# Optimization experiments

Measured on AMD Instinct MI355X. Metric: run time of the kernel, lower is better.

The kernel has to match this reference:

```python
import jax, jax.numpy as jnp
import numpy as np

N, E = 50000, 400000
IN, HID, HEADS, OUT, EDIM = 128, 16, 8, 128, 32


def _lin(key, fan_in, fan_out, bias=True):
    k1, k2 = jax.random.split(key)
    s = 1.0 / np.sqrt(fan_in)
    W = jax.random.uniform(k1, (fan_in, fan_out), jnp.float32, -s, s)
    if bias:
        b = jax.random.uniform(k2, (fan_out,), jnp.float32, -s, s)
        return W, b
    return W


def setup_inputs() -> dict:
    key = jax.random.key(0)
    ks = jax.random.split(key, 16)
    x = jax.random.normal(ks[0], (N, IN), jnp.float32)
    edge_index = jax.random.randint(ks[1], (2, E), 0, N, jnp.int64)
    edge_feats = jax.random.normal(ks[2], (E, EDIM), jnp.float32)
    H1 = HEADS * HID  # 128
    Wq1, bq1 = _lin(ks[3], IN, H1)
    Wk1, bk1 = _lin(ks[4], IN, H1)
    Wv1, bv1 = _lin(ks[5], IN, H1)
    We1 = _lin(ks[6], EDIM, H1, bias=False)
    Ws1, bs1 = _lin(ks[7], IN, H1)
    Wq2, bq2 = _lin(ks[8], H1, OUT)
    Wk2, bk2 = _lin(ks[9], H1, OUT)
    Wv2, bv2 = _lin(ks[10], H1, OUT)
    We2 = _lin(ks[11], EDIM, OUT, bias=False)
    Ws2, bs2 = _lin(ks[12], H1, OUT)
    return dict(x=x, edge_index=edge_index, edge_feats=edge_feats,
                Wq1=Wq1, bq1=bq1, Wk1=Wk1, bk1=bk1, Wv1=Wv1, bv1=bv1, We1=We1, Ws1=Ws1, bs1=bs1,
                Wq2=Wq2, bq2=bq2, Wk2=Wk2, bk2=bk2, Wv2=Wv2, bv2=bv2, We2=We2, Ws2=Ws2, bs2=bs2)


def transformer_conv(x, src, dst, e, Wq, bq, Wk, bk, Wv, bv, We, Ws, bs, heads, ch, concat):
    # PyG TransformerConv: project at nodes, gather to edges.
    n = x.shape[0]
    q = (x @ Wq + bq).reshape(n, heads, ch)[dst]          # [E,H,C]
    k = (x @ Wk + bk).reshape(n, heads, ch)[src]
    v = (x @ Wv + bv).reshape(n, heads, ch)[src]
    ee = (e @ We).reshape(-1, heads, ch)                   # edge conditioning
    k = k + ee
    v = v + ee
    alpha = (q * k).sum(-1) / jnp.sqrt(jnp.asarray(ch, x.dtype))  # [E,H]
    # per-destination segment softmax
    m = jax.ops.segment_max(alpha, dst, num_segments=n)
    m = jnp.where(jnp.isfinite(m), m, 0.0)
    ea = jnp.exp(alpha - m[dst])
    denom = jax.ops.segment_sum(ea, dst, num_segments=n)
    attn = ea / jnp.maximum(denom[dst], 1e-16)
    out = jax.ops.segment_sum(attn[:, :, None] * v, dst, num_segments=n)  # [N,H,C]
    out = out.reshape(n, heads * ch) if concat else out.mean(axis=1)
    return out + x @ Ws + bs  # root_weight skip


def reference(x, edge_index, edge_feats,
              Wq1, bq1, Wk1, bk1, Wv1, bv1, We1, Ws1, bs1,
              Wq2, bq2, Wk2, bk2, Wv2, bv2, We2, Ws2, bs2):
    src, dst = edge_index[0], edge_index[1]
    h = jax.nn.relu(transformer_conv(x, src, dst, edge_feats,
                                     Wq1, bq1, Wk1, bk1, Wv1, bv1, We1, Ws1, bs1,
                                     HEADS, HID, True))
    # dropout p=0.0 (eval) -> identity
    out = jax.nn.relu(transformer_conv(h, src, dst, edge_feats,
                                       Wq2, bq2, Wk2, bk2, Wv2, bv2, We2, Ws2, bs2,
                                       1, OUT, False))
    return out
```

## Files before the change

### kernel.cpp

```cpp
#include <hip/hip_runtime.h>


using u16 = unsigned short;
using u32 = unsigned int;

#define NODES 50000
#define EDGES 400000
#define NB196 196

typedef __attribute__((ext_vector_type(8))) short bf16x8;
typedef __attribute__((ext_vector_type(4))) float f32x4;

__device__ __forceinline__ float bflo(u32 u) { return __uint_as_float(u << 16); }
__device__ __forceinline__ float bfhi(u32 u) { return __uint_as_float(u & 0xffff0000u); }
__device__ __forceinline__ u16 f2bf(float f) {
    u32 u = __float_as_uint(f);
    u += 0x7fffu + ((u >> 16) & 1u);
    return (u16)(u >> 16);
}
__device__ __forceinline__ u32 pack2(float a, float b) {
    return (u32)f2bf(a) | ((u32)f2bf(b) << 16);
}
__device__ __forceinline__ float rdv(const void* p, int i, int f) {
    return f ? ((const float*)p)[i]
             : __uint_as_float(((u32) reinterpret_cast<const u16*>(p)[i]) << 16);
}

#if __has_builtin(__builtin_amdgcn_fdot2_f32_bf16)
typedef __attribute__((ext_vector_type(2))) __bf16 bf2;
__device__ __forceinline__ float dot2bf(u32 a, u32 b, float c) {
    return __builtin_amdgcn_fdot2_f32_bf16(__builtin_bit_cast(bf2, a),
                                           __builtin_bit_cast(bf2, b), c, false);
}
#else
__device__ __forceinline__ float dot2bf(u32 a, u32 b, float c) {
    return fmaf(bflo(a), bflo(b), fmaf(bfhi(a), bfhi(b), c));
}
#endif

__device__ __forceinline__ float fexp2(float x) {
#if __has_builtin(__builtin_amdgcn_exp2f)
    return __builtin_amdgcn_exp2f(x);
#else
    return exp2f(x);
#endif
}

template <int CTRL>
__device__ __forceinline__ float dpp_addf(float x) {
    int y = __builtin_amdgcn_update_dpp(0, __float_as_int(x), CTRL, 0xF, 0xF, true);
    return x + __int_as_float(y);
}
template <int GRP>
__device__ __forceinline__ float grp_sum(float p, int lane) {
    p = dpp_addf<0xB1>(p);
    p = dpp_addf<0x4E>(p);
    p = dpp_addf<0x141>(p);
    if (GRP == 64) {
        p = dpp_addf<0x140>(p);
        p += __int_as_float(__builtin_amdgcn_ds_swizzle(__float_as_int(p), 0x401F));
        p += __int_as_float(__builtin_amdgcn_ds_bpermute((lane ^ 32) << 2,
                                                         __float_as_int(p)));
    }
    return p;
}

template <int SRC>
__device__ __forceinline__ u32 bcast8u(u32 x) {
    return (u32)__builtin_amdgcn_ds_swizzle((int)x, 0x18 | (SRC << 5));
}

__global__ __launch_bounds__(256) void fill_sentinel(float* __restrict__ out, int n, float val) {
    int i = blockIdx.x * 256 + threadIdx.x;
    if (i < n) out[i] = val;
}

__global__ __launch_bounds__(64) void detect_fmt(const u32* __restrict__ xw,
                                                 const int* __restrict__ eraw,
                                                 int* __restrict__ flags) {
    int lane = threadIdx.x;
    u32 e = (xw[lane] >> 7) & 0xffu;
    unsigned long long sane = __ballot(e >= 90u && e <= 141u);
    unsigned long long zodd = __ballot(eraw[1 + 2 * lane] == 0);
    if (lane == 0) {
        flags[0] = (sane == ~0ull) ? 0 : 1;
        flags[1] = (zodd == ~0ull) ? 1 : 0;
    }
}

#define CXB 3125
#define CDB 1563
__global__ __launch_bounds__(256) void convert_count(
    const void* __restrict__ X, const int* __restrict__ raw,
    const int* __restrict__ flags, u16* __restrict__ xbf,
    int* __restrict__ deg, int total, int E) {
    int b = blockIdx.x;
    if (b < CXB) {
        int i = (b * 256 + threadIdx.x) * 8;
        if (i >= total) return;
        if (flags[0]) {
            const float* xf = (const float*)X + i;
            float4 lo = *reinterpret_cast<const float4*>(xf);
            float4 hi = *reinterpret_cast<const float4*>(xf + 4);
            uint4 val = make_uint4(pack2(lo.x, lo.y), pack2(lo.z, lo.w),
                                   pack2(hi.x, hi.y), pack2(hi.z, hi.w));
            *reinterpret_cast<uint4*>(xbf + i) = val;
        } else {
            *reinterpret_cast<uint4*>(xbf + i) =
                *reinterpret_cast<const uint4*>((const u16*)X + i);
        }
    } else {
        int e = (b - CXB) * 256 + threadIdx.x;
        if (e < E) {
            int f = flags[1];
            int d = f ? raw[2 * (E + e)] : raw[E + e];
            if ((unsigned)d < (unsigned)NODES) atomicAdd(&deg[d], 1);
        }
    }
}

struct TPtrs {
    const void* src[8];
    u16*        dst[8];
    int         K[8];
};
struct WqeP {
    const void *Wq1, *We1, *bq1, *Wq2, *We2, *bq2;
    u16 *WtA, *WtB, *Wt2;
    float *bqe1, *bqe2;
    uint2 *WeP1, *WeP2;
};

__global__ __launch_bounds__(256) void prep_w(TPtrs P, WqeP Q, const int* __restrict__ flags) {
    int f = flags[0];
    int b = blockIdx.x;
    if (b < 32) {
        int m = b >> 2;
        int K = P.K[m];
        int quarter = (K * 128) >> 2;
        u16* d = P.dst[m];
        int base = (b & 3) * quarter;
        const float* sf = (const float*)P.src[m];
        const u16*   sb = (const u16*)P.src[m];
        for (int idx = base + threadIdx.x; idx < base + quarter; idx += 256) {
            int k = idx >> 7, n = idx & 127;
            d[n * K + k] = f ? f2bf(sf[idx]) : sb[idx];
        }
        return;
    }
    int idx = (b - 32) * 256 + threadIdx.x;
    if (idx < 32768) {
        int col = idx >> 7, i = idx & 127;
        int hh = col >> 5, d = col & 31;
        float s = 0.f;
#pragma unroll
        for (int c = 0; c < 16; ++c)
            s += rdv(Q.Wq1, i * 128 + hh * 16 + c, f) * rdv(Q.We1, d * 128 + hh * 16 + c, f);
        if (col < 128) Q.WtA[col * 128 + i] = f2bf(s);
        else           Q.WtB[(col - 128) * 128 + i] = f2bf(s);
    } else if (idx < 49152) {
        int t = idx - 32768;
        int col = t >> 7, i = t & 127;
        float s = 0.f;
        if (col < 32) {
            for (int c = 0; c < 128; ++c)
                s += rdv(Q.Wq2, i * 128 + c, f) * rdv(Q.We2, col * 128 + c, f);
        }
        Q.Wt2[col * 128 + i] = f2bf(s * 0.125f);
    } else if (idx < 49408) {
        int col = idx - 49152;
        int hh = col >> 5, d = col & 31;
        float s = 0.f;
#pragma unroll
        for (int c = 0; c < 16; ++c)
            s += rdv(Q.bq1, hh * 16 + c, f) * rdv(Q.We1, d * 128 + hh * 16 + c, f);
        Q.bqe1[col] = s;
    } else if (idx < 49536) {
        int d = idx - 49408;
        float s = 0.f;
        if (d < 32)
            for (int c = 0; c < 128; ++c)
                s += rdv(Q.bq2, c, f) * rdv(Q.We2, d * 128 + c, f);
        Q.bqe2[d] = s * 0.125f;
    } else if (idx < 50560) {
        int ent = idx - 49536;
        int t = ent >> 6, l = ent & 63, c0 = 2 * l;
        u32 xv = pack2(rdv(Q.We1, (2 * t) * 128 + c0, f),
                       rdv(Q.We1, (2 * t + 1) * 128 + c0, f));
        u32 yv = pack2(rdv(Q.We1, (2 * t) * 128 + c0 + 1, f),
                       rdv(Q.We1, (2 * t + 1) * 128 + c0 + 1, f));
        Q.WeP1[ent] = make_uint2(xv, yv);
    } else if (idx < 51584) {
        int ent = idx - 50560;
        int t = ent >> 6, l = ent & 63, c0 = 2 * l;
        u32 xv = pack2(rdv(Q.We2, (2 * t) * 128 + c0, f),
                       rdv(Q.We2, (2 * t + 1) * 128 + c0, f));
        u32 yv = pack2(rdv(Q.We2, (2 * t) * 128 + c0 + 1, f),
                       rdv(Q.We2, (2 * t + 1) * 128 + c0 + 1, f));
        Q.WeP2[ent] = make_uint2(xv, yv);
    }
}

__device__ __forceinline__ int block_scan256(int v) {
    __shared__ int ws[4];
    int t = threadIdx.x, lane = t & 63, w = t >> 6;
    int x = v;
#pragma unroll
    for (int off = 1; off < 64; off <<= 1) {
        int y = __shfl_up(x, off, 64);
        if (lane >= off) x += y;
    }
    if (lane == 63) ws[w] = x;
    __syncthreads();
#pragma unroll
    for (int j = 0; j < 3; ++j)
        if (j < w) x += ws[j];
    return x;
}

__global__ __launch_bounds__(256) void scan_a(const int* __restrict__ deg,
                                              int* __restrict__ bsum, int n) {
    int i = blockIdx.x * 256 + threadIdx.x;
    int v = (i < n) ? deg[i] : 0;
    int incl = block_scan256(v);
    if (threadIdx.x == 255) bsum[blockIdx.x] = incl;
}

__global__ __launch_bounds__(256) void scan_b(int* __restrict__ bsum, int nb) {
    int t = threadIdx.x;
    int v = (t < nb) ? bsum[t] : 0;
    int incl = block_scan256(v);
    if (t < nb) bsum[t] = incl - v;
}

__global__ __launch_bounds__(256) void scan_c(const int* __restrict__ deg,
                                              const int* __restrict__ bsum,
                                              int* __restrict__ row_ptr,
                                              int* __restrict__ cursor, int n) {
    int b = blockIdx.x;
    int i = b * 256 + threadIdx.x;
    int v = (i < n) ? deg[i] : 0;
    int incl = block_scan256(v) + bsum[b];
    if (i < n) {
        row_ptr[i + 1] = incl;
        cursor[i] = incl - v;
    }
    if (i == 0) row_ptr[0] = 0;
}

__global__ __launch_bounds__(256) void fill_csr(const int* __restrict__ raw,
                                                const int* __restrict__ flags,
                                                int* __restrict__ cursor,
                                                int* __restrict__ srcs,
                                                int* __restrict__ eids, int E) {
    int e = blockIdx.x * 256 + threadIdx.x;
    if (e < E) {
        int f = flags[1];
        int d = f ? raw[2 * (E + e)] : raw[E + e];
        int s = f ? raw[2 * e] : raw[e];
        if ((unsigned)d < (unsigned)NODES && (unsigned)s < (unsigned)NODES) {
            int pos = atomicAdd(&cursor[d], 1);
            if ((unsigned)pos < (unsigned)E) { srcs[pos] = s; eids[pos] = e; }
        }
    }
}

__global__ __launch_bounds__(256) void gather_ef(const int* __restrict__ eids,
                                                 const void* __restrict__ EF,
                                                 const int* __restrict__ flags,
                                                 u16* __restrict__ EFG, int E) {
    int t = blockIdx.x * 256 + threadIdx.x;
    int pos = t >> 2, seg = t & 3;
    if (pos >= E) return;
    int e = eids[pos];
    uint4 val;
    if (flags[0]) {
        const float* src = (const float*)EF + (size_t)e * 32 + seg * 8;
        float4 lo = *reinterpret_cast<const float4*>(src);
        float4 hi = *reinterpret_cast<const float4*>(src + 4);
        val = make_uint4(pack2(lo.x, lo.y), pack2(lo.z, lo.w),
                         pack2(hi.x, hi.y), pack2(hi.z, hi.w));
    } else {
        val = *reinterpret_cast<const uint4*>((const u16*)EF + (size_t)e * 32 + seg * 8);
    }
    *reinterpret_cast<uint4*>(EFG + (size_t)pos * 32 + seg * 8) = val;
}

struct GemmSets {
    const u16*  Wt[6];
    const void* bias[6];
    u16*        O[6];
    int         bf32[6];
    int         pitch[6];
    float       oscale[6];
};

__global__ __launch_bounds__(256) void gemm128(
    const u16* __restrict__ A, const int* __restrict__ flags, GemmSets S, int M) {
    constexpr int K = 128;
    constexpr int PAD = K + 8;
    constexpr int KV = K / 8;
    __shared__ u16 Asl[64 * PAD];
    __shared__ u16 Bsl[128 * PAD];

    const u16*  Wt   = S.Wt[blockIdx.y];
    const void* bias = S.bias[blockIdx.y];
    u16*        O    = S.O[blockIdx.y];
    int pitch = S.pitch[blockIdx.y];
    float os  = S.oscale[blockIdx.y];
    int f = S.bf32[blockIdx.y] ? 1 : flags[0];
    int m0 = blockIdx.x * 64;

    for (int idx = threadIdx.x; idx < 64 * KV; idx += 256) {
        int r = idx / KV, cv = idx % KV;
        int gr = m0 + r;
        uint4 val = make_uint4(0, 0, 0, 0);
        if (gr < M) val = *reinterpret_cast<const uint4*>(A + (size_t)gr * K + cv * 8);
        *reinterpret_cast<uint4*>(&Asl[r * PAD + cv * 8]) = val;
    }
    for (int idx = threadIdx.x; idx < 128 * KV; idx += 256) {
        int r = idx / KV, cv = idx % KV;
        *reinterpret_cast<uint4*>(&Bsl[r * PAD + cv * 8]) =
            *reinterpret_cast<const uint4*>(Wt + r * K + cv * 8);
    }
    __syncthreads();

    int lane = threadIdx.x & 63, wv = threadIdx.x >> 6;
    int l15 = lane & 15;
    int quad = lane >> 4;
    int kq = quad * 8;

    f32x4 b4[8];
#pragma unroll
    for (int nt = 0; nt < 8; ++nt) {
        int col0 = nt * 16 + quad * 4;
        if (bias) {
            if (f) {
                b4[nt] = *reinterpret_cast<const f32x4*>((const float*)bias + col0);
            } else {
                uint2 bu = *reinterpret_cast<const uint2*>((const u16*)bias + col0);
                b4[nt][0] = bflo(bu.x); b4[nt][1] = bfhi(bu.x);
                b4[nt][2] = bflo(bu.y); b4[nt][3] = bfhi(bu.y);
            }
        } else {
            b4[nt][0] = b4[nt][1] = b4[nt][2] = b4[nt][3] = 0.f;
        }
    }

    f32x4 acc[8] = {};
#pragma unroll
    for (int k0 = 0; k0 < K; k0 += 32) {
        bf16x8 xf = *reinterpret_cast<const bf16x8*>(&Asl[(wv * 16 + l15) * PAD + k0 + kq]);
#pragma unroll
        for (int nt = 0; nt < 8; ++nt) {
            bf16x8 wf = *reinterpret_cast<const bf16x8*>(&Bsl[(nt * 16 + l15) * PAD + k0 + kq]);
            acc[nt] = __builtin_amdgcn_mfma_f32_16x16x32_bf16(wf, xf, acc[nt], 0, 0, 0);
        }
    }

    int row = m0 + wv * 16 + l15;
    if (row < M) {
        u16* Orow = O + (size_t)row * pitch;
#pragma unroll
        for (int nt = 0; nt < 8; ++nt) {
            uint2 pk;
            pk.x = pack2((acc[nt][0] + b4[nt][0]) * os, (acc[nt][1] + b4[nt][1]) * os);
            pk.y = pack2((acc[nt][2] + b4[nt][2]) * os, (acc[nt][3] + b4[nt][3]) * os);
            *reinterpret_cast<uint2*>(Orow + nt * 16 + quad * 4) = pk;
        }
    }
}

template <int HEADS, int F32OUT>
__global__ __launch_bounds__(256) void attn_kernel(
    const int* __restrict__ row_ptr, const int* __restrict__ srcs,
    const u16* __restrict__ Q, const u16* __restrict__ KV,
    const u16* __restrict__ EFG,
    const u16* __restrict__ QWA, const u16* __restrict__ QWB,
    const u16* __restrict__ SK, const uint2* __restrict__ WeP,
    void* __restrict__ OUT, int nn) {
    int wv = threadIdx.x >> 6, lane = threadIdx.x & 63;
    int node = blockIdx.x * 4 + wv;
    if (node >= nn) return;
    int h = lane >> 3, j = lane & 7;
    int c0 = lane * 2;
    constexpr int GRP = (HEADS == 8) ? 8 : 64;

    u32 qb = *reinterpret_cast<const u32*>(Q + (size_t)node * 128 + c0);
    const u16* qp = (HEADS == 8)
        ? ((h < 4 ? QWA : QWB) + (size_t)node * 128 + (h & 3) * 32 + j * 4)
        : (QWA + (size_t)node * 128 + j * 4);
    uint2 qwu = *reinterpret_cast<const uint2*>(qp);

    int beg = __builtin_amdgcn_readfirstlane(row_ptr[node]);
    int end = __builtin_amdgcn_readfirstlane(row_ptr[node + 1]);

    float l_run = 0.f, a0 = 0.f, a1 = 0.f;
    float f0 = 0.f, f1 = 0.f, f2 = 0.f, f3 = 0.f;

    auto edge_step = [&](u32 kbv, u32 vbv, uint2 ebv, bool valid) {
        float p = dot2bf(qb, kbv,
                 dot2bf(qwu.x, ebv.x,
                 dot2bf(qwu.y, ebv.y, 0.f)));
        p = grp_sum<GRP>(p, lane);
        float w = fexp2(p);
        if (!valid) w = 0.f;
        l_run += w;
        a0 = fmaf(w, bflo(vbv), a0);
        a1 = fmaf(w, bfhi(vbv), a1);
        f0 = fmaf(w, bflo(ebv.x), f0); f1 = fmaf(w, bfhi(ebv.x), f1);
        f2 = fmaf(w, bflo(ebv.y), f2); f3 = fmaf(w, bfhi(ebv.y), f3);
    };

    int i = beg;
    for (; i + 8 <= end; i += 8) {
        u32 kb[8], vb[8]; uint2 eb[8];
#pragma unroll
        for (int t = 0; t < 8; ++t) {
            int s = srcs[i + t];
            const u16* kp = KV + (size_t)s * 256;
            kb[t] = *reinterpret_cast<const u32*>(kp + c0);
            vb[t] = *reinterpret_cast<const u32*>(kp + 128 + c0);
            eb[t] = *reinterpret_cast<const uint2*>(EFG + (size_t)(i + t) * 32 + j * 4);
        }
#pragma unroll
        for (int t = 0; t < 8; ++t) edge_step(kb[t], vb[t], eb[t], true);
    }
    for (; i < end; i += 4) {
        int kleft = end - i;
        u32 kb[4], vb[4]; uint2 eb[4];
#pragma unroll
        for (int t = 0; t < 4; ++t) {
            int idx = (i + t < end) ? i + t : end - 1;
            int s = srcs[idx];
            const u16* kp = KV + (size_t)s * 256;
            kb[t] = *reinterpret_cast<const u32*>(kp + c0);
            vb[t] = *reinterpret_cast<const u32*>(kp + 128 + c0);
            eb[t] = *reinterpret_cast<const uint2*>(EFG + (size_t)idx * 32 + j * 4);
        }
#pragma unroll
        for (int t = 0; t < 4; ++t) edge_step(kb[t], vb[t], eb[t], t < kleft);
    }

    u32 Fp0 = pack2(f0, f1), Fp1 = pack2(f2, f3);
    float acc0 = 0.f, acc1 = 0.f;
#define EPI(SRC) do { \
        u32 A = bcast8u<SRC>(Fp0), B = bcast8u<SRC>(Fp1); \
        uint2 w0 = WeP[(2 * SRC) * 64 + lane]; \
        uint2 w1 = WeP[(2 * SRC + 1) * 64 + lane]; \
        acc0 = dot2bf(A, w0.x, acc0); acc0 = dot2bf(B, w1.x, acc0); \
        acc1 = dot2bf(A, w0.y, acc1); acc1 = dot2bf(B, w1.y, acc1); \
    } while (0)
    EPI(0); EPI(1); EPI(2); EPI(3); EPI(4); EPI(5); EPI(6); EPI(7);
#undef EPI

    float inv = 1.f / fmaxf(l_run, 1e-16f);
    u32 sb = *reinterpret_cast<const u32*>(SK + (size_t)node * 128 + c0);
    float o0 = fmaxf(fmaf(a0 + acc0, inv, bflo(sb)), 0.f);
    float o1 = fmaxf(fmaf(a1 + acc1, inv, bfhi(sb)), 0.f);
    if (F32OUT) {
        *reinterpret_cast<float2*>((float*)OUT + (size_t)node * 128 + c0) =
            make_float2(o0, o1);
    } else {
        *reinterpret_cast<u32*>((u16*)OUT + (size_t)node * 128 + c0) = pack2(o0, o1);
    }
}

extern "C" void kernel_launch(void* const* d_in, const int* in_sizes, int n_in,
                              void* d_out, int out_size, void* d_ws, size_t ws_size,
                              hipStream_t stream) {
    const int N = NODES, E = EDGES;
    const void* x  = d_in[0];
    const int*  ei = (const int*)d_in[1];
    const void* ef = d_in[2];
    const void* Wq1 = d_in[3];  const void* bq1 = d_in[4];
    const void* Wk1 = d_in[5];  const void* bk1 = d_in[6];
    const void* Wv1 = d_in[7];  const void* bv1 = d_in[8];
    const void* We1 = d_in[9];
    const void* Ws1 = d_in[10]; const void* bs1 = d_in[11];
    const void* Wq2 = d_in[12]; const void* bq2 = d_in[13];
    const void* Wk2 = d_in[14]; const void* bk2 = d_in[15];
    const void* Wv2 = d_in[16]; const void* bv2 = d_in[17];
    const void* We2 = d_in[18];
    const void* Ws2 = d_in[19]; const void* bs2 = d_in[20];

    char* ws = (char*)d_ws;
    size_t off = 0;
    auto carve = [&](size_t bytes) -> void* {
        void* p = ws + off;
        off += (bytes + 255) & ~(size_t)255;
        return p;
    };

    u16* WtQ1 = (u16*)carve(128 * 128 * 2);
    u16* WtK1 = (u16*)carve(128 * 128 * 2);
    u16* WtV1 = (u16*)carve(128 * 128 * 2);
    u16* WtS1 = (u16*)carve(128 * 128 * 2);
    u16* WtQ2 = (u16*)carve(128 * 128 * 2);
    u16* WtK2 = (u16*)carve(128 * 128 * 2);
    u16* WtV2 = (u16*)carve(128 * 128 * 2);
    u16* WtS2 = (u16*)carve(128 * 128 * 2);
    u16* WtqA = (u16*)carve(128 * 128 * 2);
    u16* WtqB = (u16*)carve(128 * 128 * 2);
    u16* Wtq2 = (u16*)carve(128 * 128 * 2);
    float* bqe1 = (float*)carve(256 * 4);
    float* bqe2 = (float*)carve(128 * 4);
    uint2* WeP1 = (uint2*)carve(1024 * 8);
    uint2* WeP2 = (uint2*)carve(1024 * 8);
    int* flags   = (int*)carve(256);
    int* deg     = (int*)carve((size_t)N * 4);
    int* bsum    = (int*)carve((size_t)NB196 * 4);
    int* row_ptr = (int*)carve((size_t)(N + 1) * 4);
    int* cursor  = (int*)carve((size_t)N * 4);
    int* srcs    = (int*)carve((size_t)E * 4);
    int* eids    = (int*)carve((size_t)E * 4);
    u16* xbf  = (u16*)carve((size_t)N * 128 * 2);
    u16* q    = (u16*)carve((size_t)N * 128 * 2);
    u16* kv   = (u16*)carve((size_t)N * 256 * 2);
    u16* sk   = (u16*)carve((size_t)N * 128 * 2);
    u16* h    = (u16*)carve((size_t)N * 128 * 2);
    u16* qweA = (u16*)carve((size_t)N * 128 * 2);
    u16* qweB = (u16*)carve((size_t)N * 128 * 2);
    u16* qwe2 = (u16*)carve((size_t)N * 128 * 2);
    u16* efg  = (u16*)carve((size_t)E * 32 * 2);
    const size_t REQ = off;

    if (ws_size < REQ) {
        hipLaunchKernelGGL(fill_sentinel, dim3((out_size + 255) / 256), dim3(256), 0, stream,
                           (float*)d_out, out_size, 16.0f * (float)(ws_size >> 20));
        return;
    }

    const float s2_1 = 0.25f * 1.44269504f;
    const float s2_2 = 0.08838834764831845f * 1.44269504f;

    hipLaunchKernelGGL(detect_fmt, dim3(1), dim3(64), 0, stream, (const u32*)x, ei, flags);

    (void)hipMemsetAsync(deg, 0, (size_t)N * 4, stream);
    hipLaunchKernelGGL(convert_count, dim3(CXB + CDB), dim3(256), 0, stream,
                       x, ei, flags, xbf, deg, N * 128, E);

    TPtrs tp;
    tp.src[0] = Wq1; tp.dst[0] = WtQ1; tp.K[0] = 128;
    tp.src[1] = Wk1; tp.dst[1] = WtK1; tp.K[1] = 128;
    tp.src[2] = Wv1; tp.dst[2] = WtV1; tp.K[2] = 128;
    tp.src[3] = Ws1; tp.dst[3] = WtS1; tp.K[3] = 128;
    tp.src[4] = Wq2; tp.dst[4] = WtQ2; tp.K[4] = 128;
    tp.src[5] = Wk2; tp.dst[5] = WtK2; tp.K[5] = 128;
    tp.src[6] = Wv2; tp.dst[6] = WtV2; tp.K[6] = 128;
    tp.src[7] = Ws2; tp.dst[7] = WtS2; tp.K[7] = 128;
    WqeP wp;
    wp.Wq1 = Wq1; wp.We1 = We1; wp.bq1 = bq1;
    wp.Wq2 = Wq2; wp.We2 = We2; wp.bq2 = bq2;
    wp.WtA = WtqA; wp.WtB = WtqB; wp.Wt2 = Wtq2;
    wp.bqe1 = bqe1; wp.bqe2 = bqe2;
    wp.WeP1 = WeP1; wp.WeP2 = WeP2;
    hipLaunchKernelGGL(prep_w, dim3(32 + 202), dim3(256), 0, stream, tp, wp, flags);

    hipLaunchKernelGGL(scan_a, dim3(NB196), dim3(256), 0, stream, deg, bsum, N);
    hipLaunchKernelGGL(scan_b, dim3(1), dim3(256), 0, stream, bsum, NB196);
    hipLaunchKernelGGL(scan_c, dim3(NB196), dim3(256), 0, stream, deg, bsum, row_ptr, cursor, N);
    hipLaunchKernelGGL(fill_csr, dim3((E + 255) / 256), dim3(256), 0, stream, ei, flags, cursor,
                       srcs, eids, E);

    hipLaunchKernelGGL(gather_ef, dim3(E * 4 / 256), dim3(256), 0, stream,
                       eids, ef, flags, efg, E);

    const int gN = (N + 63) / 64;
    const int gA = (N + 3) / 4;

    {
        GemmSets S;
        S.Wt[0] = WtQ1; S.bias[0] = bq1;  S.O[0] = q;        S.bf32[0] = 0; S.pitch[0] = 128; S.oscale[0] = s2_1;
        S.Wt[1] = WtK1; S.bias[1] = bk1;  S.O[1] = kv;       S.bf32[1] = 0; S.pitch[1] = 256; S.oscale[1] = 1.f;
        S.Wt[2] = WtV1; S.bias[2] = bv1;  S.O[2] = kv + 128; S.bf32[2] = 0; S.pitch[2] = 256; S.oscale[2] = 1.f;
        S.Wt[3] = WtS1; S.bias[3] = bs1;  S.O[3] = sk;       S.bf32[3] = 0; S.pitch[3] = 128; S.oscale[3] = 1.f;
        S.Wt[4] = WtqA; S.bias[4] = bqe1;       S.O[4] = qweA; S.bf32[4] = 1; S.pitch[4] = 128; S.oscale[4] = s2_1;
        S.Wt[5] = WtqB; S.bias[5] = bqe1 + 128; S.O[5] = qweB; S.bf32[5] = 1; S.pitch[5] = 128; S.oscale[5] = s2_1;
        hipLaunchKernelGGL(gemm128, dim3(gN, 6), dim3(256), 0, stream, xbf, flags, S, N);
    }
    hipLaunchKernelGGL((attn_kernel<8, 0>), dim3(gA), dim3(256), 0, stream,
                       row_ptr, srcs, q, kv, efg, qweA, qweB, sk, WeP1, (void*)h, N);

    {
        GemmSets S;
        S.Wt[0] = WtQ2; S.bias[0] = bq2;  S.O[0] = q;        S.bf32[0] = 0; S.pitch[0] = 128; S.oscale[0] = s2_2;
        S.Wt[1] = WtK2; S.bias[1] = bk2;  S.O[1] = kv;       S.bf32[1] = 0; S.pitch[1] = 256; S.oscale[1] = 1.f;
        S.Wt[2] = WtV2; S.bias[2] = bv2;  S.O[2] = kv + 128; S.bf32[2] = 0; S.pitch[2] = 256; S.oscale[2] = 1.f;
        S.Wt[3] = WtS2; S.bias[3] = bs2;  S.O[3] = sk;       S.bf32[3] = 0; S.pitch[3] = 128; S.oscale[3] = 1.f;
        S.Wt[4] = Wtq2; S.bias[4] = bqe2; S.O[4] = qwe2;     S.bf32[4] = 1; S.pitch[4] = 128; S.oscale[4] = s2_2;
        S.Wt[5] = Wtq2; S.bias[5] = bqe2; S.O[5] = qwe2;     S.bf32[5] = 1; S.pitch[5] = 128; S.oscale[5] = s2_2;
        hipLaunchKernelGGL(gemm128, dim3(gN, 5), dim3(256), 0, stream, h, flags, S, N);
    }
    hipLaunchKernelGGL((attn_kernel<1, 1>), dim3(gA), dim3(256), 0, stream,
                       row_ptr, srcs, q, kv, efg, qwe2, qwe2, sk, WeP2, d_out, N);
}
```

Baseline: 429.8 us.

## Process two destination nodes per wavefront with interleaved edge loads

The attention kernel now assigns two adjacent destination nodes to each wavefront and issues their 8-edge gather batches back to back before computing, so more memory requests are in flight per wave. The fixed 8/4 tail loops become a single clamped 8-edge loop with masking, and the edge-weight projection coefficients are loaded once and shared by both nodes' epilogues. In exchange the kernel uses more registers, which can lower occupancy, the grid has half as many waves, and lanes may idle when the two nodes have very different degrees.

```diff
diff --git a/kernel.cpp b/kernel.cpp
--- a/kernel.cpp
+++ b/kernel.cpp
@@ -371,6 +371,10 @@
     }
 }
 
+struct NState {
+    float l, a0, a1, f0, f1, f2, f3;
+};
+
 template <int HEADS, int F32OUT>
 __global__ __launch_bounds__(256) void attn_kernel(
     const int* __restrict__ row_ptr, const int* __restrict__ srcs,
@@ -380,89 +384,160 @@
     const u16* __restrict__ SK, const uint2* __restrict__ WeP,
     void* __restrict__ OUT, int nn) {
     int wv = threadIdx.x >> 6, lane = threadIdx.x & 63;
-    int node = blockIdx.x * 4 + wv;
-    if (node >= nn) return;
+    int w = blockIdx.x * 4 + wv;
+    int nA = w * 2;
+    if (nA >= nn) return;
+    bool hasB = (nA + 1) < nn;
+    int nB = hasB ? nA + 1 : nA;
     int h = lane >> 3, j = lane & 7;
     int c0 = lane * 2;
     constexpr int GRP = (HEADS == 8) ? 8 : 64;
 
-    u32 qb = *reinterpret_cast<const u32*>(Q + (size_t)node * 128 + c0);
-    const u16* qp = (HEADS == 8)
-        ? ((h < 4 ? QWA : QWB) + (size_t)node * 128 + (h & 3) * 32 + j * 4)
-        : (QWA + (size_t)node * 128 + j * 4);
-    uint2 qwu = *reinterpret_cast<const uint2*>(qp);
-
-    int beg = __builtin_amdgcn_readfirstlane(row_ptr[node]);
-    int end = __builtin_amdgcn_readfirstlane(row_ptr[node + 1]);
-
-    float l_run = 0.f, a0 = 0.f, a1 = 0.f;
-    float f0 = 0.f, f1 = 0.f, f2 = 0.f, f3 = 0.f;
-
-    auto edge_step = [&](u32 kbv, u32 vbv, uint2 ebv, bool valid) {
-        float p = dot2bf(qb, kbv,
-                 dot2bf(qwu.x, ebv.x,
-                 dot2bf(qwu.y, ebv.y, 0.f)));
-        p = grp_sum<GRP>(p, lane);
-        float w = fexp2(p);
-        if (!valid) w = 0.f;
-        l_run += w;
-        a0 = fmaf(w, bflo(vbv), a0);
-        a1 = fmaf(w, bfhi(vbv), a1);
-        f0 = fmaf(w, bflo(ebv.x), f0); f1 = fmaf(w, bfhi(ebv.x), f1);
-        f2 = fmaf(w, bflo(ebv.y), f2); f3 = fmaf(w, bfhi(ebv.y), f3);
-    };
-
-    int i = beg;
-    for (; i + 8 <= end; i += 8) {
-        u32 kb[8], vb[8]; uint2 eb[8];
+    int begA = __builtin_amdgcn_readfirstlane(row_ptr[nA]);
+    int endA = __builtin_amdgcn_readfirstlane(row_ptr[nA + 1]);
+    int endB = hasB ? __builtin_amdgcn_readfirstlane(row_ptr[nA + 2]) : endA;
+    int begB = endA;
+
+    u32 qbA = *reinterpret_cast<const u32*>(Q + (size_t)nA * 128 + c0);
+    u32 qbB = *reinterpret_cast<const u32*>(Q + (size_t)nB * 128 + c0);
+    const u16* qpA = (HEADS == 8)
+        ? ((h < 4 ? QWA : QWB) + (size_t)nA * 128 + (h & 3) * 32 + j * 4)
+        : (QWA + (size_t)nA * 128 + j * 4);
+    const u16* qpB = (HEADS == 8)
+        ? ((h < 4 ? QWA : QWB) + (size_t)nB * 128 + (h & 3) * 32 + j * 4)
+        : (QWA + (size_t)nB * 128 + j * 4);
+    uint2 qwuA = *reinterpret_cast<const uint2*>(qpA);
+    uint2 qwuB = *reinterpret_cast<const uint2*>(qpB);
+
+    auto load8 = [&](int ii, int ee, u32* kb, u32* vb, uint2* eb) {
 #pragma unroll
         for (int t = 0; t < 8; ++t) {
-            int s = srcs[i + t];
-            const u16* kp = KV + (size_t)s * 256;
-            kb[t] = *reinterpret_cast<const u32*>(kp + c0);
-            vb[t] = *reinterpret_cast<const u32*>(kp + 128 + c0);
-            eb[t] = *reinterpret_cast<const uint2*>(EFG + (size_t)(i + t) * 32 + j * 4);
-        }
-#pragma unroll
-        for (int t = 0; t < 8; ++t) edge_step(kb[t], vb[t], eb[t], true);
-    }
-    for (; i < end; i += 4) {
-        int kleft = end - i;
-        u32 kb[4], vb[4]; uint2 eb[4];
-#pragma unroll
-        for (int t = 0; t < 4; ++t) {
-            int idx = (i + t < end) ? i + t : end - 1;
+            int idx = ii + t;
+            idx = (idx < ee) ? idx : (ee - 1);
+            idx = (idx < ii) ? ii : idx;
             int s = srcs[idx];
             const u16* kp = KV + (size_t)s * 256;
             kb[t] = *reinterpret_cast<const u32*>(kp + c0);
             vb[t] = *reinterpret_cast<const u32*>(kp + 128 + c0);
             eb[t] = *reinterpret_cast<const uint2*>(EFG + (size_t)idx * 32 + j * 4);
         }
-#pragma unroll
-        for (int t = 0; t < 4; ++t) edge_step(kb[t], vb[t], eb[t], t < kleft);
-    }
-
-    u32 Fp0 = pack2(f0, f1), Fp1 = pack2(f2, f3);
-    float acc0 = 0.f, acc1 = 0.f;
-#define EPI(SRC) do { \
-        u32 A = bcast8u<SRC>(Fp0), B = bcast8u<SRC>(Fp1); \
-        uint2 w0 = WeP[(2 * SRC) * 64 + lane]; \
-        uint2 w1 = WeP[(2 * SRC + 1) * 64 + lane]; \
-        acc0 = dot2bf(A, w0.x, acc0); acc0 = dot2bf(B, w1.x, acc0); \
-        acc1 = dot2bf(A, w0.y, acc1); acc1 = dot2bf(B, w1.y, acc1); \
-    } while (0)
-    EPI(0); EPI(1); EPI(2); EPI(3); EPI(4); EPI(5); EPI(6); EPI(7);
-#undef EPI
-
-    float inv = 1.f / fmaxf(l_run, 1e-16f);
-    u32 sb = *reinterpret_cast<const u32*>(SK + (size_t)node * 128 + c0);
-    float o0 = fmaxf(fmaf(a0 + acc0, inv, bflo(sb)), 0.f);
-    float o1 = fmaxf(fmaf(a1 + acc1, inv, bfhi(sb)), 0.f);
-    if (F32OUT) {
-        *reinterpret_cast<float2*>((float*)OUT + (size_t)node * 128 + c0) =
-            make_float2(o0, o1);
-    } else {
-        *reinterpret_cast<u32*>((u16*)OUT + (size_t)node * 128 + c0) = pack2(o0, o1);
+    };
+    auto comp8 = [&](const u32* kb, const u32* vb, const uint2* eb, int kleft,
+                     u32 qb, uint2 qwu, NState& st) {
+#pragma unroll
+        for (int t = 0; t < 8; ++t) {
+            float p = dot2bf(qb, kb[t],
+                      dot2bf(qwu.x, eb[t].x,
+                      dot2bf(qwu.y, eb[t].y, 0.f)));
+            p = grp_sum<GRP>(p, lane);
+            float ww = fexp2(p);
+            if (t >= kleft) ww = 0.f;
+            st.l += ww;
+            st.a0 = fmaf(ww, bflo(vb[t]), st.a0);
+            st.a1 = fmaf(ww, bfhi(vb[t]), st.a1);
+            st.f0 = fmaf(ww, bflo(eb[t].x), st.f0);
+            st.f1 = fmaf(ww, bfhi(eb[t].x), st.f1);
+            st.f2 = fmaf(ww, bflo(eb[t].y), st.f2);
+            st.f3 = fmaf(ww, bfhi(eb[t].y), st.f3);
+        }
+    };
+
+    NState sA = {0.f, 0.f, 0.f, 0.f, 0.f, 0.f, 0.f};
+    NState sB = {0.f, 0.f, 0.f, 0.f, 0.f, 0.f, 0.f};
+
+    int iA = begA, iB = begB;
+    bool aA = iA < endA;
+    bool aB = hasB && (iB < endB);
+    while (aA || aB) {
+        u32 kbA[8], vbA[8]; uint2 ebA[8];
+        u32 kbB[8], vbB[8]; uint2 ebB[8];
+        if (aA) load8(iA, endA, kbA, vbA, ebA);
+        if (aB) load8(iB, endB, kbB, vbB, ebB);
+        if (aA) {
+            comp8(kbA, vbA, ebA, endA - iA, qbA, qwuA, sA);
+            iA += 8; aA = iA < endA;
+        }
+        if (aB) {
+            comp8(kbB, vbB, ebB, endB - iB, qbB, qwuB, sB);
+            iB += 8; aB = iB < endB;
+        }
+    }
+
+    uint2 wD[16];
+#pragma unroll
+    for (int t = 0; t < 16; ++t) wD[t] = WeP[t * 64 + lane];
+
+    auto epi = [&](const NState& st) -> float2 {
+        u32 Fp0 = pack2(st.f0, st.f1), Fp1 = pack2(st.f2, st.f3);
+        float acc0 = 0.f, acc1 = 0.f;
+        {
+            u32 A_ = bcast8u<0>(Fp0), B_ = bcast8u<0>(Fp1);
+            acc0 = dot2bf(A_, wD[0].x, acc0); acc0 = dot2bf(B_, wD[1].x, acc0);
+            acc1 = dot2bf(A_, wD[0].y, acc1); acc1 = dot2bf(B_, wD[1].y, acc1);
+        }
+        {
+            u32 A_ = bcast8u<1>(Fp0), B_ = bcast8u<1>(Fp1);
+            acc0 = dot2bf(A_, wD[2].x, acc0); acc0 = dot2bf(B_, wD[3].x, acc0);
+            acc1 = dot2bf(A_, wD[2].y, acc1); acc1 = dot2bf(B_, wD[3].y, acc1);
+        }
+        {
+            u32 A_ = bcast8u<2>(Fp0), B_ = bcast8u<2>(Fp1);
+            acc0 = dot2bf(A_, wD[4].x, acc0); acc0 = dot2bf(B_, wD[5].x, acc0);
+            acc1 = dot2bf(A_, wD[4].y, acc1); acc1 = dot2bf(B_, wD[5].y, acc1);
+        }
+        {
+            u32 A_ = bcast8u<3>(Fp0), B_ = bcast8u<3>(Fp1);
+            acc0 = dot2bf(A_, wD[6].x, acc0); acc0 = dot2bf(B_, wD[7].x, acc0);
+            acc1 = dot2bf(A_, wD[6].y, acc1); acc1 = dot2bf(B_, wD[7].y, acc1);
+        }
+        {
+            u32 A_ = bcast8u<4>(Fp0), B_ = bcast8u<4>(Fp1);
+            acc0 = dot2bf(A_, wD[8].x, acc0); acc0 = dot2bf(B_, wD[9].x, acc0);
+            acc1 = dot2bf(A_, wD[8].y, acc1); acc1 = dot2bf(B_, wD[9].y, acc1);
+        }
+        {
+            u32 A_ = bcast8u<5>(Fp0), B_ = bcast8u<5>(Fp1);
+            acc0 = dot2bf(A_, wD[10].x, acc0); acc0 = dot2bf(B_, wD[11].x, acc0);
+            acc1 = dot2bf(A_, wD[10].y, acc1); acc1 = dot2bf(B_, wD[11].y, acc1);
+        }
+        {
+            u32 A_ = bcast8u<6>(Fp0), B_ = bcast8u<6>(Fp1);
+            acc0 = dot2bf(A_, wD[12].x, acc0); acc0 = dot2bf(B_, wD[13].x, acc0);
+            acc1 = dot2bf(A_, wD[12].y, acc1); acc1 = dot2bf(B_, wD[13].y, acc1);
+        }
+        {
+            u32 A_ = bcast8u<7>(Fp0), B_ = bcast8u<7>(Fp1);
+            acc0 = dot2bf(A_, wD[14].x, acc0); acc0 = dot2bf(B_, wD[15].x, acc0);
+            acc1 = dot2bf(A_, wD[14].y, acc1); acc1 = dot2bf(B_, wD[15].y, acc1);
+        }
+        return make_float2(acc0, acc1);
+    };
+
+    {
+        float2 ee2 = epi(sA);
+        float inv = 1.f / fmaxf(sA.l, 1e-16f);
+        u32 sb = *reinterpret_cast<const u32*>(SK + (size_t)nA * 128 + c0);
+        float o0 = fmaxf(fmaf(sA.a0 + ee2.x, inv, bflo(sb)), 0.f);
+        float o1 = fmaxf(fmaf(sA.a1 + ee2.y, inv, bfhi(sb)), 0.f);
+        if (F32OUT) {
+            *reinterpret_cast<float2*>((float*)OUT + (size_t)nA * 128 + c0) =
+                make_float2(o0, o1);
+        } else {
+            *reinterpret_cast<u32*>((u16*)OUT + (size_t)nA * 128 + c0) = pack2(o0, o1);
+        }
+    }
+    if (hasB) {
+        float2 ee2 = epi(sB);
+        float inv = 1.f / fmaxf(sB.l, 1e-16f);
+        u32 sb = *reinterpret_cast<const u32*>(SK + (size_t)nB * 128 + c0);
+        float o0 = fmaxf(fmaf(sB.a0 + ee2.x, inv, bflo(sb)), 0.f);
+        float o1 = fmaxf(fmaf(sB.a1 + ee2.y, inv, bfhi(sb)), 0.f);
+        if (F32OUT) {
+            *reinterpret_cast<float2*>((float*)OUT + (size_t)nB * 128 + c0) =
+                make_float2(o0, o1);
+        } else {
+            *reinterpret_cast<u32*>((u16*)OUT + (size_t)nB * 128 + c0) = pack2(o0, o1);
+        }
     }
 }
 
@@ -567,7 +642,7 @@
                        eids, ef, flags, efg, E);
 
     const int gN = (N + 63) / 64;
-    const int gA = (N + 3) / 4;
+    const int gA = (N + 7) / 8;
 
     {
         GemmSets S;
```

New measurement: 447.9 us. 1.04x slower.

## Fuse preprocessing kernels into one cooperative persistent kernel with grid syncs

Applied to the files above, without the earlier changes.

Replaces the chain of small preprocessing launches (format detect, memset, convert/count, weight prep, three-phase scan, CSR fill, edge-feature gather) with a single cooperative kernel of 512 blocks that uses grid-wide syncs between phases. This removes per-launch overhead and inter-kernel gaps for the many tiny kernels. Grid syncs add their own cost, and a fixed 512-block grid with grid-stride loops may use the GPU less evenly than the original per-phase grids. The old multi-launch path is kept as a fallback if the cooperative launch fails.

```diff
diff --git a/kernel.cpp b/kernel.cpp
--- a/kernel.cpp
+++ b/kernel.cpp
@@ -1,5 +1,8 @@
 #include <hip/hip_runtime.h>
-
+#include <hip/hip_cooperative_groups.h>
+
+
+namespace cg = cooperative_groups;
 
 using u16 = unsigned short;
 using u32 = unsigned int;
@@ -7,6 +10,7 @@
 #define NODES 50000
 #define EDGES 400000
 #define NB196 196
+#define COOPG 512
 
 typedef __attribute__((ext_vector_type(8))) short bf16x8;
 typedef __attribute__((ext_vector_type(4))) float f32x4;
@@ -73,50 +77,6 @@
 __global__ __launch_bounds__(256) void fill_sentinel(float* __restrict__ out, int n, float val) {
     int i = blockIdx.x * 256 + threadIdx.x;
     if (i < n) out[i] = val;
-}
-
-__global__ __launch_bounds__(64) void detect_fmt(const u32* __restrict__ xw,
-                                                 const int* __restrict__ eraw,
-                                                 int* __restrict__ flags) {
-    int lane = threadIdx.x;
-    u32 e = (xw[lane] >> 7) & 0xffu;
-    unsigned long long sane = __ballot(e >= 90u && e <= 141u);
-    unsigned long long zodd = __ballot(eraw[1 + 2 * lane] == 0);
-    if (lane == 0) {
-        flags[0] = (sane == ~0ull) ? 0 : 1;
-        flags[1] = (zodd == ~0ull) ? 1 : 0;
-    }
-}
-
-#define CXB 3125
-#define CDB 1563
-__global__ __launch_bounds__(256) void convert_count(
-    const void* __restrict__ X, const int* __restrict__ raw,
-    const int* __restrict__ flags, u16* __restrict__ xbf,
-    int* __restrict__ deg, int total, int E) {
-    int b = blockIdx.x;
-    if (b < CXB) {
-        int i = (b * 256 + threadIdx.x) * 8;
-        if (i >= total) return;
-        if (flags[0]) {
-            const float* xf = (const float*)X + i;
-            float4 lo = *reinterpret_cast<const float4*>(xf);
-            float4 hi = *reinterpret_cast<const float4*>(xf + 4);
-            uint4 val = make_uint4(pack2(lo.x, lo.y), pack2(lo.z, lo.w),
-                                   pack2(hi.x, hi.y), pack2(hi.z, hi.w));
-            *reinterpret_cast<uint4*>(xbf + i) = val;
-        } else {
-            *reinterpret_cast<uint4*>(xbf + i) =
-                *reinterpret_cast<const uint4*>((const u16*)X + i);
-        }
-    } else {
-        int e = (b - CXB) * 256 + threadIdx.x;
-        if (e < E) {
-            int f = flags[1];
-            int d = f ? raw[2 * (E + e)] : raw[E + e];
-            if ((unsigned)d < (unsigned)NODES) atomicAdd(&deg[d], 1);
-        }
-    }
 }
 
 struct TPtrs {
@@ -131,24 +91,7 @@
     uint2 *WeP1, *WeP2;
 };
 
-__global__ __launch_bounds__(256) void prep_w(TPtrs P, WqeP Q, const int* __restrict__ flags) {
-    int f = flags[0];
-    int b = blockIdx.x;
-    if (b < 32) {
-        int m = b >> 2;
-        int K = P.K[m];
-        int quarter = (K * 128) >> 2;
-        u16* d = P.dst[m];
-        int base = (b & 3) * quarter;
-        const float* sf = (const float*)P.src[m];
-        const u16*   sb = (const u16*)P.src[m];
-        for (int idx = base + threadIdx.x; idx < base + quarter; idx += 256) {
-            int k = idx >> 7, n = idx & 127;
-            d[n * K + k] = f ? f2bf(sf[idx]) : sb[idx];
-        }
-        return;
-    }
-    int idx = (b - 32) * 256 + threadIdx.x;
+__device__ __forceinline__ void wqe_item(const WqeP& Q, int idx, int f) {
     if (idx < 32768) {
         int col = idx >> 7, i = idx & 127;
         int hh = col >> 5, d = col & 31;
@@ -216,6 +159,185 @@
     for (int j = 0; j < 3; ++j)
         if (j < w) x += ws[j];
     return x;
+}
+
+struct CoopArgs {
+    const void* X;
+    const int*  raw;
+    const void* EF;
+    TPtrs tp;
+    WqeP  wq;
+    int* flags;
+    int* deg; int* bsum; int* row_ptr; int* cursor;
+    int* srcs; int* eids;
+    u16* xbf; u16* efg;
+};
+
+__global__ __launch_bounds__(256) void coop_prep(CoopArgs A) {
+    cg::grid_group grid = cg::this_grid();
+    const int gid = blockIdx.x * 256 + threadIdx.x;
+    const int gsz = gridDim.x * 256;
+    const int lane = threadIdx.x & 63;
+    const int N = NODES, E = EDGES;
+
+    u32 ew = (((const u32*)A.X)[lane] >> 7) & 0xffu;
+    unsigned long long sane = __ballot(ew >= 90u && ew <= 141u);
+    unsigned long long zodd = __ballot(A.raw[1 + 2 * lane] == 0);
+    const int f  = (sane == ~0ull) ? 0 : 1;
+    const int f1 = (zodd == ~0ull) ? 1 : 0;
+    if (gid == 0) { A.flags[0] = f; A.flags[1] = f1; }
+
+    for (int i = gid; i < N; i += gsz) A.deg[i] = 0;
+    __threadfence();
+    grid.sync();
+
+    for (int i = gid; i < N * 128 / 8; i += gsz) {
+        int o = i * 8;
+        if (f) {
+            const float* xf = (const float*)A.X + o;
+            float4 lo = *reinterpret_cast<const float4*>(xf);
+            float4 hi = *reinterpret_cast<const float4*>(xf + 4);
+            *reinterpret_cast<uint4*>(A.xbf + o) =
+                make_uint4(pack2(lo.x, lo.y), pack2(lo.z, lo.w),
+                           pack2(hi.x, hi.y), pack2(hi.z, hi.w));
+        } else {
+            *reinterpret_cast<uint4*>(A.xbf + o) =
+                *reinterpret_cast<const uint4*>((const u16*)A.X + o);
+        }
+    }
+    for (int e = gid; e < E; e += gsz) {
+        int d = f1 ? A.raw[2 * (E + e)] : A.raw[E + e];
+        if ((unsigned)d < (unsigned)N) atomicAdd(&A.deg[d], 1);
+    }
+    for (int t = gid; t < 8 * 16384; t += gsz) {
+        int m = t >> 14, idx = t & 16383;
+        int k = idx >> 7, n = idx & 127;
+        const float* sf = (const float*)A.tp.src[m];
+        const u16*   sb = (const u16*)A.tp.src[m];
+        A.tp.dst[m][n * 128 + k] = f ? f2bf(sf[idx]) : sb[idx];
+    }
+    for (int idx = gid; idx < 51584; idx += gsz) wqe_item(A.wq, idx, f);
+    __threadfence();
+    grid.sync();
+
+    for (int c = blockIdx.x; c < NB196; c += gridDim.x) {
+        int i = c * 256 + threadIdx.x;
+        int v = (i < N) ? A.deg[i] : 0;
+        int incl = block_scan256(v);
+        if (threadIdx.x == 255) A.bsum[c] = incl;
+    }
+    __threadfence();
+    grid.sync();
+
+    if (blockIdx.x == 0) {
+        int t = threadIdx.x;
+        int v = (t < NB196) ? A.bsum[t] : 0;
+        int incl = block_scan256(v);
+        if (t < NB196) A.bsum[t] = incl - v;
+    }
+    __threadfence();
+    grid.sync();
+
+    for (int c = blockIdx.x; c < NB196; c += gridDim.x) {
+        int i = c * 256 + threadIdx.x;
+        int v = (i < N) ? A.deg[i] : 0;
+        int incl = block_scan256(v) + A.bsum[c];
+        if (i < N) { A.row_ptr[i + 1] = incl; A.cursor[i] = incl - v; }
+        if (i == 0) A.row_ptr[0] = 0;
+    }
+    __threadfence();
+    grid.sync();
+
+    for (int e = gid; e < E; e += gsz) {
+        int d = f1 ? A.raw[2 * (E + e)] : A.raw[E + e];
+        int s = f1 ? A.raw[2 * e] : A.raw[e];
+        if ((unsigned)d < (unsigned)N && (unsigned)s < (unsigned)N) {
+            int pos = atomicAdd(&A.cursor[d], 1);
+            if ((unsigned)pos < (unsigned)E) { A.srcs[pos] = s; A.eids[pos] = e; }
+        }
+    }
+    __threadfence();
+    grid.sync();
+
+    for (int t = gid; t < E * 4; t += gsz) {
+        int pos = t >> 2, seg = t & 3;
+        int e = A.eids[pos];
+        uint4 val;
+        if (f) {
+            const float* src = (const float*)A.EF + (size_t)e * 32 + seg * 8;
+            float4 lo = *reinterpret_cast<const float4*>(src);
+            float4 hi = *reinterpret_cast<const float4*>(src + 4);
+            val = make_uint4(pack2(lo.x, lo.y), pack2(lo.z, lo.w),
+                             pack2(hi.x, hi.y), pack2(hi.z, hi.w));
+        } else {
+            val = *reinterpret_cast<const uint4*>((const u16*)A.EF + (size_t)e * 32 + seg * 8);
+        }
+        *reinterpret_cast<uint4*>(A.efg + (size_t)pos * 32 + seg * 8) = val;
+    }
+}
+
+__global__ __launch_bounds__(64) void detect_fmt(const u32* __restrict__ xw,
+                                                 const int* __restrict__ eraw,
+                                                 int* __restrict__ flags) {
+    int lane = threadIdx.x;
+    u32 e = (xw[lane] >> 7) & 0xffu;
+    unsigned long long sane = __ballot(e >= 90u && e <= 141u);
+    unsigned long long zodd = __ballot(eraw[1 + 2 * lane] == 0);
+    if (lane == 0) {
+        flags[0] = (sane == ~0ull) ? 0 : 1;
+        flags[1] = (zodd == ~0ull) ? 1 : 0;
+    }
+}
+
+#define CXB 3125
+#define CDB 1563
+__global__ __launch_bounds__(256) void convert_count(
+    const void* __restrict__ X, const int* __restrict__ raw,
+    const int* __restrict__ flags, u16* __restrict__ xbf,
+    int* __restrict__ deg, int total, int E) {
+    int b = blockIdx.x;
+    if (b < CXB) {
+        int i = (b * 256 + threadIdx.x) * 8;
+        if (i >= total) return;
+        if (flags[0]) {
+            const float* xf = (const float*)X + i;
+            float4 lo = *reinterpret_cast<const float4*>(xf);
+            float4 hi = *reinterpret_cast<const float4*>(xf + 4);
+            uint4 val = make_uint4(pack2(lo.x, lo.y), pack2(lo.z, lo.w),
+                                   pack2(hi.x, hi.y), pack2(hi.z, hi.w));
+            *reinterpret_cast<uint4*>(xbf + i) = val;
+        } else {
+            *reinterpret_cast<uint4*>(xbf + i) =
+                *reinterpret_cast<const uint4*>((const u16*)X + i);
+        }
+    } else {
+        int e = (b - CXB) * 256 + threadIdx.x;
+        if (e < E) {
+            int f = flags[1];
+            int d = f ? raw[2 * (E + e)] : raw[E + e];
+            if ((unsigned)d < (unsigned)NODES) atomicAdd(&deg[d], 1);
+        }
+    }
+}
+
+__global__ __launch_bounds__(256) void prep_w(TPtrs P, WqeP Q, const int* __restrict__ flags) {
+    int f = flags[0];
+    int b = blockIdx.x;
+    if (b < 32) {
+        int m = b >> 2;
+        int quarter = 16384 >> 2;
+        u16* d = P.dst[m];
+        int base = (b & 3) * quarter;
+        const float* sf = (const float*)P.src[m];
+        const u16*   sb = (const u16*)P.src[m];
+        for (int idx = base + threadIdx.x; idx < base + quarter; idx += 256) {
+            int k = idx >> 7, n = idx & 127;
+            d[n * 128 + k] = f ? f2bf(sf[idx]) : sb[idx];
+        }
+        return;
+    }
+    int idx = (b - 32) * 256 + threadIdx.x;
+    if (idx < 51584) wqe_item(Q, idx, f);
 }
 
 __global__ __launch_bounds__(256) void scan_a(const int* __restrict__ deg,
@@ -534,12 +656,6 @@
     const float s2_1 = 0.25f * 1.44269504f;
     const float s2_2 = 0.08838834764831845f * 1.44269504f;
 
-    hipLaunchKernelGGL(detect_fmt, dim3(1), dim3(64), 0, stream, (const u32*)x, ei, flags);
-
-    (void)hipMemsetAsync(deg, 0, (size_t)N * 4, stream);
-    hipLaunchKernelGGL(convert_count, dim3(CXB + CDB), dim3(256), 0, stream,
-                       x, ei, flags, xbf, deg, N * 128, E);
-
     TPtrs tp;
     tp.src[0] = Wq1; tp.dst[0] = WtQ1; tp.K[0] = 128;
     tp.src[1] = Wk1; tp.dst[1] = WtK1; tp.K[1] = 128;
@@ -555,16 +671,32 @@
     wp.WtA = WtqA; wp.WtB = WtqB; wp.Wt2 = Wtq2;
     wp.bqe1 = bqe1; wp.bqe2 = bqe2;
     wp.WeP1 = WeP1; wp.WeP2 = WeP2;
-    hipLaunchKernelGGL(prep_w, dim3(32 + 202), dim3(256), 0, stream, tp, wp, flags);
-
-    hipLaunchKernelGGL(scan_a, dim3(NB196), dim3(256), 0, stream, deg, bsum, N);
-    hipLaunchKernelGGL(scan_b, dim3(1), dim3(256), 0, stream, bsum, NB196);
-    hipLaunchKernelGGL(scan_c, dim3(NB196), dim3(256), 0, stream, deg, bsum, row_ptr, cursor, N);
-    hipLaunchKernelGGL(fill_csr, dim3((E + 255) / 256), dim3(256), 0, stream, ei, flags, cursor,
-                       srcs, eids, E);
-
-    hipLaunchKernelGGL(gather_ef, dim3(E * 4 / 256), dim3(256), 0, stream,
-                       eids, ef, flags, efg, E);
+
+    CoopArgs ca;
+    ca.X = x; ca.raw = ei; ca.EF = ef;
+    ca.tp = tp; ca.wq = wp;
+    ca.flags = flags;
+    ca.deg = deg; ca.bsum = bsum; ca.row_ptr = row_ptr; ca.cursor = cursor;
+    ca.srcs = srcs; ca.eids = eids;
+    ca.xbf = xbf; ca.efg = efg;
+    void* kargs[] = { &ca };
+    hipError_t cerr = hipLaunchCooperativeKernel(
+        reinterpret_cast<void*>(coop_prep), dim3(COOPG), dim3(256), kargs, 0, stream);
+    if (cerr != hipSuccess) {
+        hipLaunchKernelGGL(detect_fmt, dim3(1), dim3(64), 0, stream, (const u32*)x, ei, flags);
+        (void)hipMemsetAsync(deg, 0, (size_t)N * 4, stream);
+        hipLaunchKernelGGL(convert_count, dim3(CXB + CDB), dim3(256), 0, stream,
+                           x, ei, flags, xbf, deg, N * 128, E);
+        hipLaunchKernelGGL(prep_w, dim3(32 + 202), dim3(256), 0, stream, tp, wp, flags);
+        hipLaunchKernelGGL(scan_a, dim3(NB196), dim3(256), 0, stream, deg, bsum, N);
+        hipLaunchKernelGGL(scan_b, dim3(1), dim3(256), 0, stream, bsum, NB196);
+        hipLaunchKernelGGL(scan_c, dim3(NB196), dim3(256), 0, stream, deg, bsum, row_ptr,
+                           cursor, N);
+        hipLaunchKernelGGL(fill_csr, dim3((E + 255) / 256), dim3(256), 0, stream, ei, flags,
+                           cursor, srcs, eids, E);
+        hipLaunchKernelGGL(gather_ef, dim3(E * 4 / 256), dim3(256), 0, stream,
+                           eids, ef, flags, efg, E);
+    }
 
     const int gN = (N + 63) / 64;
     const int gA = (N + 3) / 4;
```

New measurement: 1.072 ms. 2.49x slower.
